# Performance work log

Measured on AMD Instinct MI355X. Metric: run time of the kernel, lower is better.

Reference implementation:

```python
import jax, jax.numpy as jnp
import numpy as np

N_HEADS = 16

def setup_inputs() -> dict:
    key = jax.random.key(0)
    ks = jax.random.split(key, 5)
    B, T, C = 4, 2048, 1024
    x = jax.random.normal(ks[0], (B, T, C), dtype=jnp.float32)
    w_qkv = jax.random.normal(ks[1], (C, 3 * C), dtype=jnp.float32) * (C ** -0.5)
    b_qkv = jnp.zeros((3 * C,), dtype=jnp.float32)
    w_proj = jax.random.normal(ks[2], (C, C), dtype=jnp.float32) * (C ** -0.5)
    b_proj = jnp.zeros((C,), dtype=jnp.float32)
    return {"x": x, "w_qkv": w_qkv, "b_qkv": b_qkv, "w_proj": w_proj, "b_proj": b_proj}


def reference(x, w_qkv, b_qkv, w_proj, b_proj):
    B, T, C = x.shape
    H = N_HEADS
    hd = C // H
    scale = hd ** -0.5
    qkv = x @ w_qkv + b_qkv                      # [B,T,3C]
    q, k, v = jnp.split(qkv, 3, axis=-1)         # each [B,T,C]
    # -> [B,H,T,hd]
    q = q.reshape(B, T, H, hd).transpose(0, 2, 1, 3)
    k = k.reshape(B, T, H, hd).transpose(0, 2, 1, 3)
    v = v.reshape(B, T, H, hd).transpose(0, 2, 1, 3)
    attn = jnp.einsum("bhqd,bhkd->bhqk", q, k) * scale
    causal = jnp.tril(jnp.ones((T, T), dtype=bool))
    attn = jnp.where(causal, attn, -jnp.inf)
    attn = jax.nn.softmax(attn, axis=-1)         # dropout p=0 in eval/reference
    out = jnp.einsum("bhqk,bhkd->bhqd", attn, v)
    out = out.transpose(0, 2, 1, 3).reshape(B, T, C)
    return out @ w_proj + b_proj
```

## Files before the change

kernel.cpp:

```cpp
#include <hip/hip_runtime.h>
#include <hip/hip_bf16.h>


typedef float f32x4 __attribute__((ext_vector_type(4)));
typedef float f32x16 __attribute__((ext_vector_type(16)));
typedef __bf16 bf16x8 __attribute__((ext_vector_type(8)));
typedef short short8v __attribute__((ext_vector_type(8)));
typedef unsigned int u32x4 __attribute__((ext_vector_type(4)));

__device__ __forceinline__ unsigned short f2bf(float f) {
  __hip_bfloat16 h = __float2bfloat16(f);
  return __builtin_bit_cast(unsigned short, h);
}

__device__ __forceinline__ void glds16(const void* g, void* l) {
  __builtin_amdgcn_global_load_lds((const __attribute__((address_space(1))) void*)g,
                                   (__attribute__((address_space(3))) void*)l, 16, 0, 0);
}

__global__ void cvt_f32_bf16_kernel(const float* __restrict__ in,
                                    unsigned short* __restrict__ out, int n) {
  int stride = gridDim.x * blockDim.x * 4;
  for (int i = (blockIdx.x * blockDim.x + threadIdx.x) * 4; i < n; i += stride) {
    float4 v = *(const float4*)(in + i);
    ushort4 o;
    o.x = f2bf(v.x); o.y = f2bf(v.y); o.z = f2bf(v.z); o.w = f2bf(v.w);
    *(ushort4*)(out + i) = o;
  }
}

__global__ void transpose_cvt_kernel(const float* __restrict__ in,
                                     unsigned short* __restrict__ out, int K, int N) {
  __shared__ unsigned short tile[32][33];
  int tx = threadIdx.x & 31, ty = threadIdx.x >> 5;
  int n0 = blockIdx.x * 32, k0 = blockIdx.y * 32;
#pragma unroll
  for (int i = 0; i < 32; i += 8)
    tile[ty + i][tx] = f2bf(in[(size_t)(k0 + ty + i) * N + n0 + tx]);
  __syncthreads();
#pragma unroll
  for (int i = 0; i < 32; i += 8)
    out[(size_t)(n0 + ty + i) * K + k0 + tx] = tile[tx][ty + i];
}

template <int OUT_F32>
__global__ __launch_bounds__(256) void gemm_bt_kernel(
    const unsigned short* __restrict__ A, const unsigned short* __restrict__ Bt,
    const float* __restrict__ bias, void* __restrict__ Cv, int M, int N, int K) {
  __shared__ unsigned short sA[128 * 32];
  __shared__ unsigned short sB[128 * 32];
  int tid = threadIdx.x;
  int lane = tid & 63, wid = tid >> 6;
  int g = lane >> 4, r16 = lane & 15;
  int m0 = blockIdx.y * 128, n0 = blockIdx.x * 128;
  int wm = wid >> 1, wn = wid & 1;
  f32x4 acc[4][4] = {};
  int srow = tid >> 2, scol = (tid & 3) * 8;
  const unsigned short* Ap0 = A + (size_t)(m0 + srow) * K + scol;
  const unsigned short* Ap1 = A + (size_t)(m0 + 64 + srow) * K + scol;
  const unsigned short* Bp0 = Bt + (size_t)(n0 + srow) * K + scol;
  const unsigned short* Bp1 = Bt + (size_t)(n0 + 64 + srow) * K + scol;
  unsigned short* la0 = sA + tid * 8;
  unsigned short* la1 = sA + 2048 + tid * 8;
  unsigned short* lb0 = sB + tid * 8;
  unsigned short* lb1 = sB + 2048 + tid * 8;
  for (int kt = 0; kt < K; kt += 32) {
    glds16(Ap0 + kt, la0);
    glds16(Ap1 + kt, la1);
    glds16(Bp0 + kt, lb0);
    glds16(Bp1 + kt, lb1);
    __syncthreads();
    bf16x8 af[4], bfr[4];
#pragma unroll
    for (int m = 0; m < 4; ++m)
      af[m] = *(const bf16x8*)&sA[(wm * 64 + m * 16 + r16) * 32 + g * 8];
#pragma unroll
    for (int n = 0; n < 4; ++n)
      bfr[n] = *(const bf16x8*)&sB[(wn * 64 + n * 16 + r16) * 32 + g * 8];
#pragma unroll
    for (int m = 0; m < 4; ++m)
#pragma unroll
      for (int n = 0; n < 4; ++n)
        acc[m][n] = __builtin_amdgcn_mfma_f32_16x16x32_bf16(af[m], bfr[n], acc[m][n], 0, 0, 0);
    __syncthreads();
  }
#pragma unroll
  for (int m = 0; m < 4; ++m)
#pragma unroll
    for (int n = 0; n < 4; ++n)
#pragma unroll
      for (int r = 0; r < 4; ++r) {
        int row = m0 + wm * 64 + m * 16 + g * 4 + r;
        int col = n0 + wn * 64 + n * 16 + r16;
        float v = acc[m][n][r] + bias[col];
        if (OUT_F32)
          ((float*)Cv)[(size_t)row * N + col] = v;
        else
          ((unsigned short*)Cv)[(size_t)row * N + col] = f2bf(v);
      }
}

__global__ void transpose_v_kernel(const unsigned short* __restrict__ qkv,
                                   unsigned short* __restrict__ vT) {
  __shared__ unsigned short tl[64][80];
  int t0 = blockIdx.x * 64;
  int bh = blockIdx.y, b = bh >> 4, h = bh & 15;
  int tid = threadIdx.x;
  int row = tid >> 2, c0 = (tid & 3) * 16;
  const unsigned short* src =
      qkv + (size_t)(b * 2048 + t0 + row) * 3072 + 2048 + h * 64 + c0;
  short8v a0 = *(const short8v*)src;
  short8v a1 = *(const short8v*)(src + 8);
#pragma unroll
  for (int j = 0; j < 8; ++j) tl[c0 + j][row] = (unsigned short)a0[j];
#pragma unroll
  for (int j = 0; j < 8; ++j) tl[c0 + 8 + j][row] = (unsigned short)a1[j];
  __syncthreads();
  int d = tid >> 2, tc = (tid & 3) * 16;
  unsigned short* dst = vT + (size_t)(bh * 64 + d) * 2048 + t0 + tc;
  *(short8v*)dst = *(const short8v*)&tl[d][tc];
  *(short8v*)(dst + 8) = *(const short8v*)&tl[d][tc + 8];
}

__global__ __launch_bounds__(512, 4) void attn_kernel(
    const unsigned short* __restrict__ qkv, const unsigned short* __restrict__ vT,
    unsigned short* __restrict__ ao) {
  __shared__ unsigned short sK[2][4096];
  __shared__ unsigned short sV[2][4096];
  __shared__ float lbuf[8][32];
  const int T = 2048, C3 = 3072;
  const float K1 = 23.083120654223415f;
  const float K2 = 16158.66f;
  int x = blockIdx.x;
  int xcd = x & 7, rest = x >> 3;
  int bh = xcd * 8 + (rest & 7);
  int qt = 7 - (rest >> 3);
  int b = bh >> 4, h = bh & 15;
  int tid = threadIdx.x, lane = tid & 63, w = tid >> 6;
  int l31 = lane & 31, hi = lane >> 5;

  int c = tid;
  int row = c >> 3, oct = (c & 7) ^ (row & 7);
  const unsigned short* Kb = qkv + (size_t)(b * T + row) * C3 + 1024 + h * 64 + oct * 8;
  const unsigned short* Vb = vT + (size_t)(bh * 64 + row) * 2048 + oct * 8;

  auto STAGE = [&](int buf, int kt) {
    int kv0 = kt * 64;
    glds16(Kb + (size_t)kv0 * C3, &sK[buf][c * 8]);
    glds16(Vb + kv0, &sV[buf][c * 8]);
  };

  int wq0 = qt * 256 + w * 32;

  const unsigned short* qp = qkv + (size_t)(b * T + wq0 + l31) * C3 + h * 64;
  bf16x8 qf[4];
#pragma unroll
  for (int d0 = 0; d0 < 4; ++d0)
    qf[d0] = *(const bf16x8*)(qp + d0 * 16 + hi * 8);

  u32x4 onesw = {0x3F803F80u, 0x3F803F80u, 0x3F803F80u, 0x3F803F80u};
  bf16x8 vones = __builtin_bit_cast(bf16x8, onesw);

  f32x16 o[2] = {};
  f32x16 lacc = {};

  int nkv = 4 * qt + 4;
  STAGE(0, 0);
  __syncthreads();
  int cur = 0;
#pragma unroll 1
  for (int kt = 0; kt < nkv; ++kt) {
    if (kt + 1 < nkv) STAGE(cur ^ 1, kt + 1);
    int kv0 = kt * 64;
    if (kv0 <= wq0 + 31) {
      f32x16 s[2] = {};
      __builtin_amdgcn_s_setprio(1);
#pragma unroll
      for (int d0 = 0; d0 < 4; ++d0) {
        int oc = ((d0 * 2 + hi) ^ (l31 & 7)) * 8;
        bf16x8 kf0 = *(const bf16x8*)&sK[cur][l31 * 64 + oc];
        bf16x8 kf1 = *(const bf16x8*)&sK[cur][(32 + l31) * 64 + oc];
        s[0] = __builtin_amdgcn_mfma_f32_32x32x16_bf16(kf0, qf[d0], s[0], 0, 0, 0);
        s[1] = __builtin_amdgcn_mfma_f32_32x32x16_bf16(kf1, qf[d0], s[1], 0, 0, 0);
      }
      __builtin_amdgcn_s_setprio(0);

      if (kv0 + 63 > wq0) {
        int thr = wq0 + l31 - kv0 - 4 * hi;
#pragma unroll
        for (int sub = 0; sub < 2; ++sub)
#pragma unroll
          for (int r = 0; r < 16; ++r) {
            int cc = sub * 32 + (r & 3) + 8 * (r >> 2);
            s[sub][r] = (cc <= thr) ? s[sub][r] : -3e38f;
          }
      }

      int pb[2][16];
#pragma unroll
      for (int sub = 0; sub < 2; ++sub)
#pragma unroll
        for (int r = 0; r < 16; ++r)
          pb[sub][r] = (int)fmaxf(fmaf(s[sub][r], K1, K2), 0.0f);

      unsigned int pk[2][8];
#pragma unroll
      for (int sub = 0; sub < 2; ++sub)
#pragma unroll
        for (int i = 0; i < 8; ++i)
          pk[sub][i] = __builtin_amdgcn_perm((unsigned)pb[sub][2 * i + 1],
                                             (unsigned)pb[sub][2 * i], 0x05040100u);
      unsigned int rc[2][4];
#pragma unroll
      for (int sub = 0; sub < 2; ++sub) {
        unsigned int s0 = hi ? pk[sub][0] : pk[sub][2];
        unsigned int s1 = hi ? pk[sub][1] : pk[sub][3];
        unsigned int s2 = hi ? pk[sub][4] : pk[sub][6];
        unsigned int s3 = hi ? pk[sub][5] : pk[sub][7];
        rc[sub][0] = __shfl_xor(s0, 32, 64);
        rc[sub][1] = __shfl_xor(s1, 32, 64);
        rc[sub][2] = __shfl_xor(s2, 32, 64);
        rc[sub][3] = __shfl_xor(s3, 32, 64);
      }

      __builtin_amdgcn_s_setprio(1);
#pragma unroll
      for (int sub = 0; sub < 2; ++sub)
#pragma unroll
        for (int t = 0; t < 2; ++t) {
          u32x4 av;
          av.x = hi ? rc[sub][2 * t]     : pk[sub][4 * t];
          av.y = hi ? rc[sub][2 * t + 1] : pk[sub][4 * t + 1];
          av.z = hi ? pk[sub][4 * t + 2] : rc[sub][2 * t];
          av.w = hi ? pk[sub][4 * t + 3] : rc[sub][2 * t + 1];
          bf16x8 pa = __builtin_bit_cast(bf16x8, av);
          int kvs = sub * 2 + t;
          int ocv = ((kvs * 2 + hi) ^ (l31 & 7)) * 8;
          bf16x8 vf0 = *(const bf16x8*)&sV[cur][l31 * 64 + ocv];
          bf16x8 vf1 = *(const bf16x8*)&sV[cur][(32 + l31) * 64 + ocv];
          o[0] = __builtin_amdgcn_mfma_f32_32x32x16_bf16(pa, vf0, o[0], 0, 0, 0);
          o[1] = __builtin_amdgcn_mfma_f32_32x32x16_bf16(pa, vf1, o[1], 0, 0, 0);
          lacc = __builtin_amdgcn_mfma_f32_32x32x16_bf16(pa, vones, lacc, 0, 0, 0);
        }
      __builtin_amdgcn_s_setprio(0);
    }
    __syncthreads();
    cur ^= 1;
  }

  if (l31 == 0) {
#pragma unroll
    for (int r = 0; r < 16; ++r)
      lbuf[w][(r & 3) + 8 * (r >> 2) + 4 * hi] = lacc[r];
  }
  __syncthreads();
  float inv = 1.f / lbuf[w][l31];
#pragma unroll
  for (int r = 0; r < 16; ++r) {
    int qrow = (r & 3) + 8 * (r >> 2) + 4 * hi;
    float iv = __shfl(inv, qrow, 64);
    size_t base = (size_t)(b * T + wq0 + qrow) * 1024 + h * 64 + l31;
    ao[base] = f2bf(o[0][r] * iv);
    ao[base + 32] = f2bf(o[1][r] * iv);
  }
}

extern "C" void kernel_launch(void* const* d_in, const int* in_sizes, int n_in,
                              void* d_out, int out_size, void* d_ws, size_t ws_size,
                              hipStream_t stream) {
  const float* x      = (const float*)d_in[0];
  const float* w_qkv  = (const float*)d_in[1];
  const float* b_qkv  = (const float*)d_in[2];
  const float* w_proj = (const float*)d_in[3];
  const float* b_proj = (const float*)d_in[4];
  float* out = (float*)d_out;

  char* ws = (char*)d_ws;
  unsigned short* xb     = (unsigned short*)(ws);
  unsigned short* ao     = (unsigned short*)(ws);
  unsigned short* wqkvT  = (unsigned short*)(ws + (16u << 20));
  unsigned short* wprojT = (unsigned short*)(ws + (22u << 20));
  unsigned short* qkv    = (unsigned short*)(ws + (24u << 20));
  unsigned short* vT     = (unsigned short*)(ws + (72u << 20));

  cvt_f32_bf16_kernel<<<2048, 256, 0, stream>>>(x, xb, 8192 * 1024);
  transpose_cvt_kernel<<<dim3(3072 / 32, 1024 / 32), 256, 0, stream>>>(w_qkv, wqkvT, 1024, 3072);
  transpose_cvt_kernel<<<dim3(1024 / 32, 1024 / 32), 256, 0, stream>>>(w_proj, wprojT, 1024, 1024);

  gemm_bt_kernel<0><<<dim3(3072 / 128, 8192 / 128), 256, 0, stream>>>(
      xb, wqkvT, b_qkv, (void*)qkv, 8192, 3072, 1024);

  transpose_v_kernel<<<dim3(32, 64), 256, 0, stream>>>(qkv, vT);

  attn_kernel<<<dim3(512), 512, 0, stream>>>(qkv, vT, ao);

  gemm_bt_kernel<1><<<dim3(1024 / 128, 8192 / 128), 256, 0, stream>>>(
      ao, wprojT, b_proj, (void*)out, 8192, 1024, 1024);
}
```

Baseline: 187.0 us.

## Triple-buffer GEMM LDS tiles with async global-to-LDS prefetch

The bf16 GEMM kernel now uses three LDS buffers for the A and B tiles and prefetches two K-steps ahead with global_load_lds. Manual vmcnt waits and one barrier per iteration replace the two __syncthreads, so global loads overlap the MFMA work. This triples LDS usage per block, which may lower occupancy, and it relies on the vmcnt counts matching exactly the four loads issued per stage.

```diff
diff --git a/kernel.cpp b/kernel.cpp
--- a/kernel.cpp
+++ b/kernel.cpp
@@ -47,8 +47,8 @@
 __global__ __launch_bounds__(256) void gemm_bt_kernel(
     const unsigned short* __restrict__ A, const unsigned short* __restrict__ Bt,
     const float* __restrict__ bias, void* __restrict__ Cv, int M, int N, int K) {
-  __shared__ unsigned short sA[128 * 32];
-  __shared__ unsigned short sB[128 * 32];
+  __shared__ unsigned short sA[3][128 * 32];
+  __shared__ unsigned short sB[3][128 * 32];
   int tid = threadIdx.x;
   int lane = tid & 63, wid = tid >> 6;
   int g = lane >> 4, r16 = lane & 15;
@@ -60,29 +60,46 @@
   const unsigned short* Ap1 = A + (size_t)(m0 + 64 + srow) * K + scol;
   const unsigned short* Bp0 = Bt + (size_t)(n0 + srow) * K + scol;
   const unsigned short* Bp1 = Bt + (size_t)(n0 + 64 + srow) * K + scol;
-  unsigned short* la0 = sA + tid * 8;
-  unsigned short* la1 = sA + 2048 + tid * 8;
-  unsigned short* lb0 = sB + tid * 8;
-  unsigned short* lb1 = sB + 2048 + tid * 8;
-  for (int kt = 0; kt < K; kt += 32) {
-    glds16(Ap0 + kt, la0);
-    glds16(Ap1 + kt, la1);
-    glds16(Bp0 + kt, lb0);
-    glds16(Bp1 + kt, lb1);
-    __syncthreads();
+
+  auto STAGE = [&](int buf, int kt) {
+    glds16(Ap0 + kt, &sA[buf][tid * 8]);
+    glds16(Ap1 + kt, &sA[buf][2048 + tid * 8]);
+    glds16(Bp0 + kt, &sB[buf][tid * 8]);
+    glds16(Bp1 + kt, &sB[buf][2048 + tid * 8]);
+  };
+
+  int nt = K >> 5;
+  STAGE(0, 0);
+  STAGE(1, 32);
+  int cur = 0;
+#pragma unroll 1
+  for (int t = 0; t < nt; ++t) {
+    if (t + 1 < nt) {
+      asm volatile("s_waitcnt vmcnt(4)" ::: "memory");
+    } else {
+      asm volatile("s_waitcnt vmcnt(0)" ::: "memory");
+    }
+    __builtin_amdgcn_s_barrier();
+    __builtin_amdgcn_sched_barrier(0);
+    if (t + 2 < nt) {
+      int nb = cur + 2; if (nb >= 3) nb -= 3;
+      STAGE(nb, (t + 2) * 32);
+    }
+    const unsigned short* a = sA[cur];
+    const unsigned short* bb = sB[cur];
     bf16x8 af[4], bfr[4];
 #pragma unroll
     for (int m = 0; m < 4; ++m)
-      af[m] = *(const bf16x8*)&sA[(wm * 64 + m * 16 + r16) * 32 + g * 8];
+      af[m] = *(const bf16x8*)&a[(wm * 64 + m * 16 + r16) * 32 + g * 8];
 #pragma unroll
     for (int n = 0; n < 4; ++n)
-      bfr[n] = *(const bf16x8*)&sB[(wn * 64 + n * 16 + r16) * 32 + g * 8];
+      bfr[n] = *(const bf16x8*)&bb[(wn * 64 + n * 16 + r16) * 32 + g * 8];
 #pragma unroll
     for (int m = 0; m < 4; ++m)
 #pragma unroll
       for (int n = 0; n < 4; ++n)
         acc[m][n] = __builtin_amdgcn_mfma_f32_16x16x32_bf16(af[m], bfr[n], acc[m][n], 0, 0, 0);
-    __syncthreads();
+    cur = cur < 2 ? cur + 1 : 0;
   }
 #pragma unroll
   for (int m = 0; m < 4; ++m)
```

After: 178.1 us. 1.05x faster.
